# Performance work log

Measured on AMD Instinct MI355X. Metric: run time of the kernel, lower is better.

Reference implementation:

```python
import jax, jax.numpy as jnp
import numpy as np
from jax import lax

N = 40       # num_users
K = 20       # num_channels
F = 3        # num_features (conv length dim)
SS = K * N   # state_size = 800
B = 16384


def _conv1d(x, w, b):
    # x: [B, C_in, L], w: [C_out, C_in, 3], SAME padding (pad=1)
    y = lax.conv_general_dilated(x, w, window_strides=(1,), padding=[(1, 1)],
                                 dimension_numbers=('NCH', 'OIH', 'NCH'))
    return y + b[None, :, None]


def _get_mask(state):
    # state: [B, SS, F]; status feature is index 2 (== -1 since F=3)
    visited = state[:, :, 2] != 0.0                      # [B, SS]
    vm = visited.reshape(B, K, N)                        # [B, K, N] (flat idx = chan*N + user)
    user_any = vm.any(axis=1)                            # [B, N]: user visited on any channel
    chan_full = vm.sum(axis=2) >= 2                      # [B, K]: channel has >=2 users
    mask = visited \
        | jnp.broadcast_to(user_any[:, None, :], (B, K, N)).reshape(B, SS) \
        | jnp.broadcast_to(chan_full[:, :, None], (B, K, N)).reshape(B, SS)
    return mask


def setup_inputs() -> dict:
    key = jax.random.key(0)
    ks = jax.random.split(key, 12)
    state = jax.random.normal(ks[0], (B, SS, F), jnp.float32)
    keep = jax.random.bernoulli(ks[1], 0.02, (B, SS)).astype(jnp.float32)
    state = state.at[:, :, 2].multiply(keep)
    s = 0.02
    w1 = jax.random.normal(ks[2], (128, SS, 3), jnp.float32) * s
    b1 = jnp.zeros((128,), jnp.float32)
    w2 = jax.random.normal(ks[3], (256, 128, 3), jnp.float32) * s
    b2 = jnp.zeros((256,), jnp.float32)
    w3 = jax.random.normal(ks[4], (128, 256, 3), jnp.float32) * s
    b3 = jnp.zeros((128,), jnp.float32)
    wl1 = jax.random.normal(ks[5], (64 * F, 128 * F), jnp.float32) * s   # [192, 384]
    bl1 = jnp.zeros((64 * F,), jnp.float32)
    wl2 = jax.random.normal(ks[6], (SS, 64 * F), jnp.float32) * s        # [800, 192]
    bl2 = jnp.zeros((SS,), jnp.float32)
    return {"state": state, "w1": w1, "b1": b1, "w2": w2, "b2": b2,
            "w3": w3, "b3": b3, "wl1": wl1, "bl1": bl1, "wl2": wl2, "bl2": bl2}


def reference(state, w1, b1, w2, b2, w3, b3, wl1, bl1, wl2, bl2):
    mask = _get_mask(state)
    x = jax.nn.relu(_conv1d(state, w1, b1))   # [B,128,3]
    x = jax.nn.relu(_conv1d(x, w2, b2))       # [B,256,3]
    x = jax.nn.relu(_conv1d(x, w3, b3))       # [B,128,3]
    x = x.reshape(B, -1)                      # [B,384]
    x = jax.nn.relu(x @ wl1.T + bl1)          # [B,192]
    out = x @ wl2.T + bl2                     # [B,800]
    return jnp.where(mask, -jnp.inf, out)
```

## Files before the change

kernel.cpp:

```cpp
#include <hip/hip_runtime.h>
#include <cstdint>
#include <cstddef>
#include <math.h>

typedef short bf16x8 __attribute__((ext_vector_type(8)));
typedef float f32x4 __attribute__((ext_vector_type(4)));
typedef unsigned long long u64;

#define NEG_HUGE (-3.0e38f)

__device__ __forceinline__ ushort f2bf(float x) {
    union { float f; uint32_t u; } a; a.f = x;
    uint32_t r = a.u + 0x7FFF + ((a.u >> 16) & 1);
    return (ushort)(r >> 16);
}

__device__ __forceinline__ void gload_lds16(const void* g, void* l) {
    __builtin_amdgcn_global_load_lds(
        (const __attribute__((address_space(1))) uint32_t*)g,
        (__attribute__((address_space(3))) uint32_t*)l, 16, 0, 0);
}

#define SCHED() __builtin_amdgcn_sched_barrier(0)
#define SBAR() do { SCHED(); __builtin_amdgcn_s_barrier(); SCHED(); } while (0)

__device__ __forceinline__ ushort conv_elem(const float* __restrict__ w,
                                            int Cin, int idx, int Kpad) {
    int n = idx / Kpad, k = idx - n * Kpad;
    float val = 0.f;
    if (k < Cin * 3) {
        int co = n / 3, l = n % 3, ci = k / 3, lx = k % 3;
        int t = lx - l + 1;
        if (t >= 0 && t < 3) val = w[(co * Cin + ci) * 3 + t];
    }
    return f2bf(val);
}

__device__ __forceinline__ ushort lin_elem(const float* __restrict__ wl,
                                           int K, int Nreal, int idx) {
    int n = idx / K, k = idx - n * K;
    return (n < Nreal) ? f2bf(wl[n * K + k]) : (ushort)0;
}

__global__ void prep_all(const float* __restrict__ w1, const float* __restrict__ w2,
                         const float* __restrict__ w3, const float* __restrict__ wl1,
                         const float* __restrict__ wl2,
                         ushort* __restrict__ W1T, ushort* __restrict__ W2T,
                         ushort* __restrict__ W3T, ushort* __restrict__ WL1T,
                         ushort* __restrict__ WL2T) {
    int idx = blockIdx.x * 256 + threadIdx.x;
    if (idx < 933888) {
        W1T[idx] = conv_elem(w1, 800, idx, 2432);
        return;
    }
    idx -= 933888;
    if (idx < 294912) {
        W2T[idx] = conv_elem(w2, 128, idx, 384);
        return;
    }
    idx -= 294912;
    if (idx < 294912) {
        W3T[idx] = conv_elem(w3, 256, idx, 768);
        return;
    }
    idx -= 294912;
    if (idx < 73728) {
        WL1T[idx] = lin_elem(wl1, 384, 192, idx);
        return;
    }
    idx -= 73728;
    if (idx < 184320) {
        WL2T[idx] = lin_elem(wl2, 192, 800, idx);
    }
}

__global__ __launch_bounds__(512, 4)
void conv1_kernel(const float* __restrict__ state, const ushort* __restrict__ W1T,
                  const float* __restrict__ b1, ushort* __restrict__ X1g,
                  uint32_t* __restrict__ maskg)
{
    extern __shared__ char lds[];
    char* BF0 = lds;
    char* BF1 = lds + 8192;
    char* Wb0 = lds + 16384;
    char* Wb1 = lds + 40960;
    uint32_t* maskw = (uint32_t*)(lds + 65536);

    const int tid = threadIdx.x, lane = tid & 63, wid = tid >> 6;
    const int m0 = blockIdx.x * 64;
    const int n0 = blockIdx.y * 192;
    const bool domask = (blockIdx.y == 0);
    const int ml = lane & 15, kq = lane >> 4;
    const int mbase = (wid >> 2) * 32;
    const int wn0 = (wid & 3) * 48;

    const int srow = tid >> 3, seg = tid & 7;
    const float* sbase = state + (size_t)(m0 + srow) * 2400 + seg * 8;

    f32x4 acc[3][2];
    #pragma unroll
    for (int f = 0; f < 3; ++f)
        #pragma unroll
        for (int mi = 0; mi < 2; ++mi) acc[f][mi] = (f32x4){0.f, 0.f, 0.f, 0.f};

    auto loadS = [&](float4 (&sv)[2], int c) {
        int kb = c * 64 + seg * 8;
        if (kb < 2400) {
            sv[0] = *(const float4*)(sbase + c * 64);
            sv[1] = *(const float4*)(sbase + c * 64 + 4);
        } else {
            sv[0] = (float4){0.f, 0.f, 0.f, 0.f};
            sv[1] = (float4){0.f, 0.f, 0.f, 0.f};
        }
    };
    auto stage_write = [&](float4 (&sv)[2], int c, char* dst) {
        float fv[8] = {sv[0].x, sv[0].y, sv[0].z, sv[0].w,
                       sv[1].x, sv[1].y, sv[1].z, sv[1].w};
        bf16x8 h;
        #pragma unroll
        for (int j = 0; j < 8; ++j) h[j] = (short)f2bf(fv[j]);
        *(bf16x8*)(dst + srow * 128 + ((seg * 16) ^ ((srow & 7) << 4))) = h;
        if (domask) {
            int kbase = c * 64 + seg * 8;
            int kmod = kbase % 3;
            uint32_t* mrow = &maskw[srow * 25];
            #define MCHK(J) { if (fv[J] != 0.0f) { int a = (kbase + (J)) / 3; \
                              atomicOr(&mrow[a >> 5], 1u << (a & 31)); } }
            if (kmod == 0)      { MCHK(2) MCHK(5) }
            else if (kmod == 1) { MCHK(1) MCHK(4) MCHK(7) }
            else                { MCHK(0) MCHK(3) MCHK(6) }
            #undef MCHK
        }
    };
    auto loadW = [&](int c, char* dst) {
        #pragma unroll
        for (int i = 0; i < 3; ++i) {
            int s = i * 512 + tid;
            int r = s >> 3, o8 = s & 7;
            gload_lds16(W1T + (size_t)(n0 + r) * 2432 + c * 64 + ((o8 ^ (r & 7)) * 8),
                        dst + s * 16);
        }
    };
    auto mfmaC = [&](const char* wb, const char* sb) {
        #pragma unroll
        for (int ks = 0; ks < 2; ++ks) {
            bf16x8 af[3], bv[2];
            #pragma unroll
            for (int f = 0; f < 3; ++f) {
                int n = wn0 + f * 16 + ml;
                af[f] = *(const bf16x8*)(wb + n * 128 + (((ks * 4 + kq) * 16) ^ ((n & 7) << 4)));
            }
            #pragma unroll
            for (int mi = 0; mi < 2; ++mi) {
                int m = mbase + mi * 16 + ml;
                bv[mi] = *(const bf16x8*)(sb + m * 128 + (((ks * 4 + kq) * 16) ^ ((m & 7) << 4)));
            }
            #pragma unroll
            for (int f = 0; f < 3; ++f)
                #pragma unroll
                for (int mi = 0; mi < 2; ++mi)
                    acc[f][mi] = __builtin_amdgcn_mfma_f32_16x16x32_bf16(af[f], bv[mi], acc[f][mi], 0, 0, 0);
        }
    };

    for (int i = tid; i < 64 * 25; i += 512) maskw[i] = 0;
    float4 svA[2], svB[2];
    loadS(svA, 0);
    loadW(0, Wb0);
    loadS(svB, 1);
    SCHED();
    asm volatile("s_waitcnt lgkmcnt(0)" ::: "memory");
    SBAR();

    #define BODY(SV, C, SB, WBC, WBN) do {                                   \
        stage_write(SV, (C), SB);                                            \
        SCHED();                                                             \
        asm volatile("s_waitcnt lgkmcnt(0)" ::: "memory");                   \
        SBAR();                                                              \
        loadW(((C) + 1 > 37) ? 37 : (C) + 1, WBN);                           \
        loadS(SV, ((C) + 2 > 37) ? 37 : (C) + 2);                            \
        SCHED();                                                             \
        asm volatile("s_waitcnt vmcnt(7)" ::: "memory");                     \
        SBAR();                                                              \
        mfmaC(WBC, SB);                                                      \
    } while (0)

    #pragma unroll 1
    for (int p = 0; p < 19; ++p) {
        BODY(svA, 2 * p,     BF0, Wb0, Wb1);
        BODY(svB, 2 * p + 1, BF1, Wb1, Wb0);
    }
    #undef BODY

    asm volatile("s_waitcnt vmcnt(0) lgkmcnt(0)" ::: "memory");
    SBAR();

    {
        const int nq4 = (lane >> 4) * 4;
        #pragma unroll
        for (int f = 0; f < 3; ++f) {
            int n4 = n0 + wn0 + f * 16 + nq4;
            float bv0 = b1[n4 / 3], bv1 = b1[(n4 + 1) / 3];
            float bv2 = b1[(n4 + 2) / 3], bv3 = b1[(n4 + 3) / 3];
            #pragma unroll
            for (int mi = 0; mi < 2; ++mi) {
                int m = mbase + mi * 16 + ml;
                ushort4 o;
                o.x = f2bf(fmaxf(acc[f][mi][0] + bv0, 0.f));
                o.y = f2bf(fmaxf(acc[f][mi][1] + bv1, 0.f));
                o.z = f2bf(fmaxf(acc[f][mi][2] + bv2, 0.f));
                o.w = f2bf(fmaxf(acc[f][mi][3] + bv3, 0.f));
                *(ushort4*)(X1g + (size_t)(m0 + m) * 384 + n4) = o;
            }
        }
    }

    if (domask && tid < 64) {
        uint32_t* mw = &maskw[tid * 25];
        const u64 M40 = (1ull << 40) - 1;
        u64 ua = 0; uint32_t cf = 0;
        #pragma unroll
        for (int g = 0; g < 5; ++g) {
            uint32_t w0 = mw[5*g], w1 = mw[5*g+1], w2 = mw[5*g+2], w3 = mw[5*g+3], w4 = mw[5*g+4];
            u64 c0 = ( (u64)w0        | ((u64)w1 << 32)) & M40;
            u64 c1 = (((u64)w1 >> 8)  | ((u64)w2 << 24)) & M40;
            u64 c2 = (((u64)w2 >> 16) | ((u64)w3 << 16)) & M40;
            u64 c3 = (((u64)w3 >> 24) | ((u64)w4 << 8))  & M40;
            ua |= c0 | c1 | c2 | c3;
            if (__popcll(c0) >= 2) cf |= 1u << (4*g);
            if (__popcll(c1) >= 2) cf |= 1u << (4*g+1);
            if (__popcll(c2) >= 2) cf |= 1u << (4*g+2);
            if (__popcll(c3) >= 2) cf |= 1u << (4*g+3);
        }
        uint32_t* mg = maskg + (size_t)(m0 + tid) * 25;
        #pragma unroll
        for (int g = 0; g < 5; ++g) {
            uint32_t w0 = mw[5*g], w1 = mw[5*g+1], w2 = mw[5*g+2], w3 = mw[5*g+3], w4 = mw[5*g+4];
            u64 c0 = ( (u64)w0        | ((u64)w1 << 32)) & M40;
            u64 c1 = (((u64)w1 >> 8)  | ((u64)w2 << 24)) & M40;
            u64 c2 = (((u64)w2 >> 16) | ((u64)w3 << 16)) & M40;
            u64 c3 = (((u64)w3 >> 24) | ((u64)w4 << 8))  & M40;
            u64 m0v = c0 | ua | (((cf >> (4*g))     & 1u) ? M40 : 0ull);
            u64 m1v = c1 | ua | (((cf >> (4*g + 1)) & 1u) ? M40 : 0ull);
            u64 m2v = c2 | ua | (((cf >> (4*g + 2)) & 1u) ? M40 : 0ull);
            u64 m3v = c3 | ua | (((cf >> (4*g + 3)) & 1u) ? M40 : 0ull);
            mg[5*g]   = (uint32_t)m0v;
            mg[5*g+1] = (uint32_t)(m0v >> 32) | (uint32_t)(m1v << 8);
            mg[5*g+2] = (uint32_t)(m1v >> 24) | (uint32_t)(m2v << 16);
            mg[5*g+3] = (uint32_t)(m2v >> 16) | (uint32_t)(m3v << 24);
            mg[5*g+4] = (uint32_t)(m3v >> 8);
        }
    }
}

template<int K, bool BDIV3, bool RELU, bool F32OUT>
__global__ __launch_bounds__(512, 4)
void glayer3(const ushort* __restrict__ Ag, const ushort* __restrict__ WTg,
             const float* __restrict__ bias, void* __restrict__ Yg, int ldy,
             const uint32_t* __restrict__ maskg)
{
    constexpr int MF = 4, NF = 3;
    constexpr int MT = 128, NT = 192;
    constexpr int NC = K / 64;
    constexpr int ABYTES = MT * 128;
    constexpr int WBYTES = NT * 128;
    static_assert(NC >= 3, "pipeline assumes >=3 chunks");
    extern __shared__ char lds[];

    const int tid = threadIdx.x, lane = tid & 63, wid = tid >> 6;
    const int m0 = blockIdx.x * MT;
    const int n0 = blockIdx.y * NT;
    const int ml = lane & 15, kq = lane >> 4;
    const int mw = wid >> 2, nw = wid & 3;
    const int mbase = mw * MF * 16;
    const int wn0 = nw * NF * 16;

    f32x4 acc[NF][MF];
    #pragma unroll
    for (int f = 0; f < NF; ++f)
        #pragma unroll
        for (int mi = 0; mi < MF; ++mi) acc[f][mi] = (f32x4){0.f, 0.f, 0.f, 0.f};

    auto stage = [&](int c, int b) {
        char* Ab = lds + b * ABYTES;
        char* Wb = lds + 2 * ABYTES + b * WBYTES;
        #pragma unroll
        for (int i = 0; i < 2; ++i) {
            int s = i * 512 + tid;
            int r = s >> 3, o8 = s & 7;
            gload_lds16(Ag + (size_t)(m0 + r) * K + c * 64 + ((o8 ^ (r & 7)) * 8),
                        Ab + s * 16);
        }
        #pragma unroll
        for (int i = 0; i < 3; ++i) {
            int s = i * 512 + tid;
            int r = s >> 3, o8 = s & 7;
            gload_lds16(WTg + (size_t)(n0 + r) * K + c * 64 + ((o8 ^ (r & 7)) * 8),
                        Wb + s * 16);
        }
    };
    auto mfmaC = [&](int b) {
        const char* Ab = lds + b * ABYTES;
        const char* Wb = lds + 2 * ABYTES + b * WBYTES;
        #pragma unroll
        for (int ks = 0; ks < 2; ++ks) {
            bf16x8 af[NF], bv[MF];
            #pragma unroll
            for (int f = 0; f < NF; ++f) {
                int n = wn0 + f * 16 + ml;
                af[f] = *(const bf16x8*)(Wb + n * 128 + (((ks * 4 + kq) * 16) ^ ((n & 7) << 4)));
            }
            #pragma unroll
            for (int mi = 0; mi < MF; ++mi) {
                int m = mbase + mi * 16 + ml;
                bv[mi] = *(const bf16x8*)(Ab + m * 128 + (((ks * 4 + kq) * 16) ^ ((m & 7) << 4)));
            }
            #pragma unroll
            for (int f = 0; f < NF; ++f)
                #pragma unroll
                for (int mi = 0; mi < MF; ++mi)
                    acc[f][mi] = __builtin_amdgcn_mfma_f32_16x16x32_bf16(af[f], bv[mi], acc[f][mi], 0, 0, 0);
        }
    };

    stage(0, 0);
    stage(1, 1);
    asm volatile("s_waitcnt vmcnt(5)" ::: "memory");
    SBAR();

    #pragma unroll 1
    for (int c = 0; c < NC; ++c) {
        mfmaC(c & 1);
        if (c + 2 < NC) {
            SBAR();
            stage(c + 2, c & 1);
            asm volatile("s_waitcnt vmcnt(5)" ::: "memory");
            SBAR();
        } else if (c + 1 < NC) {
            SBAR();
            asm volatile("s_waitcnt vmcnt(0)" ::: "memory");
            SBAR();
        }
    }

    const int nq4 = (lane >> 4) * 4;
    if (!F32OUT) {
        ushort* Y = (ushort*)Yg;
        #pragma unroll
        for (int f = 0; f < NF; ++f) {
            int n4 = n0 + wn0 + f * 16 + nq4;
            float bv0 = bias[BDIV3 ? n4 / 3 : n4];
            float bv1 = bias[BDIV3 ? (n4 + 1) / 3 : n4 + 1];
            float bv2 = bias[BDIV3 ? (n4 + 2) / 3 : n4 + 2];
            float bv3 = bias[BDIV3 ? (n4 + 3) / 3 : n4 + 3];
            #pragma unroll
            for (int mi = 0; mi < MF; ++mi) {
                int m = mbase + mi * 16 + ml;
                float x0 = acc[f][mi][0] + bv0, x1 = acc[f][mi][1] + bv1;
                float x2 = acc[f][mi][2] + bv2, x3 = acc[f][mi][3] + bv3;
                if (RELU) { x0 = fmaxf(x0, 0.f); x1 = fmaxf(x1, 0.f);
                            x2 = fmaxf(x2, 0.f); x3 = fmaxf(x3, 0.f); }
                ushort4 o = {f2bf(x0), f2bf(x1), f2bf(x2), f2bf(x3)};
                *(ushort4*)(Y + (size_t)(m0 + m) * ldy + n4) = o;
            }
        }
    } else {
        float* Y = (float*)Yg;
        #pragma unroll
        for (int f = 0; f < NF; ++f) {
            int nf = n0 + wn0 + f * 16;
            if (nf < 800) {
                int n4 = nf + nq4, sh = n4 & 31;
                float bv0 = bias[n4], bv1 = bias[n4 + 1];
                float bv2 = bias[n4 + 2], bv3 = bias[n4 + 3];
                #pragma unroll
                for (int mi = 0; mi < MF; ++mi) {
                    int m = mbase + mi * 16 + ml;
                    uint32_t mwv = maskg[(size_t)(m0 + m) * 25 + (nf >> 5)];
                    float4 v;
                    v.x = ((mwv >> (sh + 0)) & 1u) ? NEG_HUGE : (acc[f][mi][0] + bv0);
                    v.y = ((mwv >> (sh + 1)) & 1u) ? NEG_HUGE : (acc[f][mi][1] + bv1);
                    v.z = ((mwv >> (sh + 2)) & 1u) ? NEG_HUGE : (acc[f][mi][2] + bv2);
                    v.w = ((mwv >> (sh + 3)) & 1u) ? NEG_HUGE : (acc[f][mi][3] + bv3);
                    *(float4*)(Y + (size_t)(m0 + m) * ldy + n4) = v;
                }
            }
        }
    }
}

__global__ void ws_fail_kernel(float* out) {
    if (threadIdx.x == 0 && blockIdx.x == 0) out[0] = NAN;
}

extern "C" void kernel_launch(void* const* d_in, const int* in_sizes, int n_in,
                              void* d_out, int out_size, void* d_ws, size_t ws_size,
                              hipStream_t stream) {
    const float* state = (const float*)d_in[0];
    const float* w1  = (const float*)d_in[1];
    const float* b1  = (const float*)d_in[2];
    const float* w2  = (const float*)d_in[3];
    const float* b2  = (const float*)d_in[4];
    const float* w3  = (const float*)d_in[5];
    const float* b3  = (const float*)d_in[6];
    const float* wl1 = (const float*)d_in[7];
    const float* bl1 = (const float*)d_in[8];
    const float* wl2 = (const float*)d_in[9];
    const float* bl2 = (const float*)d_in[10];
    float* out = (float*)d_out;

    char* ws = (char*)d_ws;
    size_t off = 0;
    auto carve = [&](size_t bytes) {
        char* p = ws + off;
        off = (off + bytes + 255) & ~(size_t)255;
        return p;
    };
    ushort* W1T  = (ushort*)carve(384ull * 2432 * 2);
    ushort* W2T  = (ushort*)carve(768ull * 384 * 2);
    ushort* W3T  = (ushort*)carve(384ull * 768 * 2);
    ushort* WL1T = (ushort*)carve(192ull * 384 * 2);
    ushort* WL2T = (ushort*)carve(960ull * 192 * 2);
    ushort* X1g  = (ushort*)carve(16384ull * 384 * 2);
    ushort* X2g  = (ushort*)carve(16384ull * 768 * 2);
    ushort* X3g  = (ushort*)carve(16384ull * 384 * 2);
    ushort* X4g  = (ushort*)carve(16384ull * 192 * 2);
    uint32_t* maskg = (uint32_t*)carve(16384ull * 25 * 4);

    if (off > ws_size) {
        ws_fail_kernel<<<1, 64, 0, stream>>>(out);
        return;
    }

    prep_all<<<(1781760 + 255) / 256, 256, 0, stream>>>(w1, w2, w3, wl1, wl2,
                                                        W1T, W2T, W3T, WL1T, WL2T);

    (void)hipFuncSetAttribute(reinterpret_cast<const void*>(conv1_kernel),
                        hipFuncAttributeMaxDynamicSharedMemorySize, 71936);
    conv1_kernel<<<dim3(256, 2), 512, 71936, stream>>>(state, W1T, b1, X1g, maskg);

    auto kc2 = glayer3<384, true, true, false>;
    (void)hipFuncSetAttribute(reinterpret_cast<const void*>(kc2),
                        hipFuncAttributeMaxDynamicSharedMemorySize, 81920);
    kc2<<<dim3(128, 4), 512, 81920, stream>>>(X1g, W2T, b2, X2g, 768, nullptr);

    auto kc3 = glayer3<768, true, true, false>;
    (void)hipFuncSetAttribute(reinterpret_cast<const void*>(kc3),
                        hipFuncAttributeMaxDynamicSharedMemorySize, 81920);
    kc3<<<dim3(128, 2), 512, 81920, stream>>>(X2g, W3T, b3, X3g, 384, nullptr);

    auto kc4 = glayer3<384, false, true, false>;
    (void)hipFuncSetAttribute(reinterpret_cast<const void*>(kc4),
                        hipFuncAttributeMaxDynamicSharedMemorySize, 81920);
    kc4<<<dim3(128, 1), 512, 81920, stream>>>(X3g, WL1T, bl1, X4g, 192, nullptr);

    auto kc5 = glayer3<192, false, false, true>;
    (void)hipFuncSetAttribute(reinterpret_cast<const void*>(kc5),
                        hipFuncAttributeMaxDynamicSharedMemorySize, 81920);
    kc5<<<dim3(128, 5), 512, 81920, stream>>>(X4g, WL2T, bl2, out, 800, maskg);
}
```

Baseline: 132.6 us.

## Shrink conv1 N-tile to 128 and move mask finalization into layer-2 kernel

Conv1's output tile shrinks from 192 to 128 columns, so the grid grows to three column blocks, the LDS footprint drops to 48KB and the occupancy hint rises to 6 blocks per CU. The per-block LDS mask staging is removed: mask bits are OR'd atomically straight into global memory, which prep_all now zeroes. The user-any and channel-full finalization moves into the epilogue of the conv2 kernel. This lowers conv1 register and LDS pressure and raises parallelism, at the cost of global atomics in place of LDS atomics and an extra pass over W1T tiles.

```diff
diff --git a/kernel.cpp b/kernel.cpp
--- a/kernel.cpp
+++ b/kernel.cpp
@@ -47,34 +47,22 @@
                          const float* __restrict__ wl2,
                          ushort* __restrict__ W1T, ushort* __restrict__ W2T,
                          ushort* __restrict__ W3T, ushort* __restrict__ WL1T,
-                         ushort* __restrict__ WL2T) {
+                         ushort* __restrict__ WL2T, uint32_t* __restrict__ maskg) {
     int idx = blockIdx.x * 256 + threadIdx.x;
-    if (idx < 933888) {
-        W1T[idx] = conv_elem(w1, 800, idx, 2432);
-        return;
-    }
+    if (idx < 933888) { W1T[idx] = conv_elem(w1, 800, idx, 2432); return; }
     idx -= 933888;
-    if (idx < 294912) {
-        W2T[idx] = conv_elem(w2, 128, idx, 384);
-        return;
-    }
+    if (idx < 294912) { W2T[idx] = conv_elem(w2, 128, idx, 384); return; }
     idx -= 294912;
-    if (idx < 294912) {
-        W3T[idx] = conv_elem(w3, 256, idx, 768);
-        return;
-    }
+    if (idx < 294912) { W3T[idx] = conv_elem(w3, 256, idx, 768); return; }
     idx -= 294912;
-    if (idx < 73728) {
-        WL1T[idx] = lin_elem(wl1, 384, 192, idx);
-        return;
-    }
+    if (idx < 73728)  { WL1T[idx] = lin_elem(wl1, 384, 192, idx); return; }
     idx -= 73728;
-    if (idx < 184320) {
-        WL2T[idx] = lin_elem(wl2, 192, 800, idx);
-    }
-}
-
-__global__ __launch_bounds__(512, 4)
+    if (idx < 184320) { WL2T[idx] = lin_elem(wl2, 192, 800, idx); return; }
+    idx -= 184320;
+    if (idx < 409600) maskg[idx] = 0;
+}
+
+__global__ __launch_bounds__(512, 6)
 void conv1_kernel(const float* __restrict__ state, const ushort* __restrict__ W1T,
                   const float* __restrict__ b1, ushort* __restrict__ X1g,
                   uint32_t* __restrict__ maskg)
@@ -83,23 +71,22 @@
     char* BF0 = lds;
     char* BF1 = lds + 8192;
     char* Wb0 = lds + 16384;
-    char* Wb1 = lds + 40960;
-    uint32_t* maskw = (uint32_t*)(lds + 65536);
+    char* Wb1 = lds + 32768;
 
     const int tid = threadIdx.x, lane = tid & 63, wid = tid >> 6;
     const int m0 = blockIdx.x * 64;
-    const int n0 = blockIdx.y * 192;
+    const int n0 = blockIdx.y * 128;
     const bool domask = (blockIdx.y == 0);
     const int ml = lane & 15, kq = lane >> 4;
     const int mbase = (wid >> 2) * 32;
-    const int wn0 = (wid & 3) * 48;
+    const int wn0 = (wid & 3) * 32;
 
     const int srow = tid >> 3, seg = tid & 7;
     const float* sbase = state + (size_t)(m0 + srow) * 2400 + seg * 8;
 
-    f32x4 acc[3][2];
+    f32x4 acc[2][2];
     #pragma unroll
-    for (int f = 0; f < 3; ++f)
+    for (int f = 0; f < 2; ++f)
         #pragma unroll
         for (int mi = 0; mi < 2; ++mi) acc[f][mi] = (f32x4){0.f, 0.f, 0.f, 0.f};
 
@@ -123,7 +110,7 @@
         if (domask) {
             int kbase = c * 64 + seg * 8;
             int kmod = kbase % 3;
-            uint32_t* mrow = &maskw[srow * 25];
+            uint32_t* mrow = maskg + (size_t)(m0 + srow) * 25;
             #define MCHK(J) { if (fv[J] != 0.0f) { int a = (kbase + (J)) / 3; \
                               atomicOr(&mrow[a >> 5], 1u << (a & 31)); } }
             if (kmod == 0)      { MCHK(2) MCHK(5) }
@@ -134,7 +121,7 @@
     };
     auto loadW = [&](int c, char* dst) {
         #pragma unroll
-        for (int i = 0; i < 3; ++i) {
+        for (int i = 0; i < 2; ++i) {
             int s = i * 512 + tid;
             int r = s >> 3, o8 = s & 7;
             gload_lds16(W1T + (size_t)(n0 + r) * 2432 + c * 64 + ((o8 ^ (r & 7)) * 8),
@@ -144,9 +131,9 @@
     auto mfmaC = [&](const char* wb, const char* sb) {
         #pragma unroll
         for (int ks = 0; ks < 2; ++ks) {
-            bf16x8 af[3], bv[2];
-            #pragma unroll
-            for (int f = 0; f < 3; ++f) {
+            bf16x8 af[2], bv[2];
+            #pragma unroll
+            for (int f = 0; f < 2; ++f) {
                 int n = wn0 + f * 16 + ml;
                 af[f] = *(const bf16x8*)(wb + n * 128 + (((ks * 4 + kq) * 16) ^ ((n & 7) << 4)));
             }
@@ -156,14 +143,13 @@
                 bv[mi] = *(const bf16x8*)(sb + m * 128 + (((ks * 4 + kq) * 16) ^ ((m & 7) << 4)));
             }
             #pragma unroll
-            for (int f = 0; f < 3; ++f)
+            for (int f = 0; f < 2; ++f)
                 #pragma unroll
                 for (int mi = 0; mi < 2; ++mi)
                     acc[f][mi] = __builtin_amdgcn_mfma_f32_16x16x32_bf16(af[f], bv[mi], acc[f][mi], 0, 0, 0);
         }
     };
 
-    for (int i = tid; i < 64 * 25; i += 512) maskw[i] = 0;
     float4 svA[2], svB[2];
     loadS(svA, 0);
     loadW(0, Wb0);
@@ -180,7 +166,7 @@
         loadW(((C) + 1 > 37) ? 37 : (C) + 1, WBN);                           \
         loadS(SV, ((C) + 2 > 37) ? 37 : (C) + 2);                            \
         SCHED();                                                             \
-        asm volatile("s_waitcnt vmcnt(7)" ::: "memory");                     \
+        asm volatile("s_waitcnt vmcnt(6)" ::: "memory");                     \
         SBAR();                                                              \
         mfmaC(WBC, SB);                                                      \
     } while (0)
@@ -198,7 +184,7 @@
     {
         const int nq4 = (lane >> 4) * 4;
         #pragma unroll
-        for (int f = 0; f < 3; ++f) {
+        for (int f = 0; f < 2; ++f) {
             int n4 = n0 + wn0 + f * 16 + nq4;
             float bv0 = b1[n4 / 3], bv1 = b1[(n4 + 1) / 3];
             float bv2 = b1[(n4 + 2) / 3], bv3 = b1[(n4 + 3) / 3];
@@ -214,50 +200,13 @@
             }
         }
     }
-
-    if (domask && tid < 64) {
-        uint32_t* mw = &maskw[tid * 25];
-        const u64 M40 = (1ull << 40) - 1;
-        u64 ua = 0; uint32_t cf = 0;
-        #pragma unroll
-        for (int g = 0; g < 5; ++g) {
-            uint32_t w0 = mw[5*g], w1 = mw[5*g+1], w2 = mw[5*g+2], w3 = mw[5*g+3], w4 = mw[5*g+4];
-            u64 c0 = ( (u64)w0        | ((u64)w1 << 32)) & M40;
-            u64 c1 = (((u64)w1 >> 8)  | ((u64)w2 << 24)) & M40;
-            u64 c2 = (((u64)w2 >> 16) | ((u64)w3 << 16)) & M40;
-            u64 c3 = (((u64)w3 >> 24) | ((u64)w4 << 8))  & M40;
-            ua |= c0 | c1 | c2 | c3;
-            if (__popcll(c0) >= 2) cf |= 1u << (4*g);
-            if (__popcll(c1) >= 2) cf |= 1u << (4*g+1);
-            if (__popcll(c2) >= 2) cf |= 1u << (4*g+2);
-            if (__popcll(c3) >= 2) cf |= 1u << (4*g+3);
-        }
-        uint32_t* mg = maskg + (size_t)(m0 + tid) * 25;
-        #pragma unroll
-        for (int g = 0; g < 5; ++g) {
-            uint32_t w0 = mw[5*g], w1 = mw[5*g+1], w2 = mw[5*g+2], w3 = mw[5*g+3], w4 = mw[5*g+4];
-            u64 c0 = ( (u64)w0        | ((u64)w1 << 32)) & M40;
-            u64 c1 = (((u64)w1 >> 8)  | ((u64)w2 << 24)) & M40;
-            u64 c2 = (((u64)w2 >> 16) | ((u64)w3 << 16)) & M40;
-            u64 c3 = (((u64)w3 >> 24) | ((u64)w4 << 8))  & M40;
-            u64 m0v = c0 | ua | (((cf >> (4*g))     & 1u) ? M40 : 0ull);
-            u64 m1v = c1 | ua | (((cf >> (4*g + 1)) & 1u) ? M40 : 0ull);
-            u64 m2v = c2 | ua | (((cf >> (4*g + 2)) & 1u) ? M40 : 0ull);
-            u64 m3v = c3 | ua | (((cf >> (4*g + 3)) & 1u) ? M40 : 0ull);
-            mg[5*g]   = (uint32_t)m0v;
-            mg[5*g+1] = (uint32_t)(m0v >> 32) | (uint32_t)(m1v << 8);
-            mg[5*g+2] = (uint32_t)(m1v >> 24) | (uint32_t)(m2v << 16);
-            mg[5*g+3] = (uint32_t)(m2v >> 16) | (uint32_t)(m3v << 24);
-            mg[5*g+4] = (uint32_t)(m3v >> 8);
-        }
-    }
 }
 
 template<int K, bool BDIV3, bool RELU, bool F32OUT>
 __global__ __launch_bounds__(512, 4)
 void glayer3(const ushort* __restrict__ Ag, const ushort* __restrict__ WTg,
              const float* __restrict__ bias, void* __restrict__ Yg, int ldy,
-             const uint32_t* __restrict__ maskg)
+             const uint32_t* __restrict__ maskg, uint32_t* __restrict__ fin_mask)
 {
     constexpr int MF = 4, NF = 3;
     constexpr int MT = 128, NT = 192;
@@ -387,6 +336,45 @@
             }
         }
     }
+
+    if (fin_mask && blockIdx.y == 0 && tid < 128) {
+        uint32_t* mw = fin_mask + (size_t)(m0 + tid) * 25;
+        uint32_t w[25];
+        #pragma unroll
+        for (int i = 0; i < 25; ++i) w[i] = mw[i];
+        const u64 M40 = (1ull << 40) - 1;
+        u64 ua = 0; uint32_t cf = 0;
+        #pragma unroll
+        for (int g = 0; g < 5; ++g) {
+            uint32_t w0 = w[5*g], w1 = w[5*g+1], w2 = w[5*g+2], w3 = w[5*g+3], w4 = w[5*g+4];
+            u64 c0 = ( (u64)w0        | ((u64)w1 << 32)) & M40;
+            u64 c1 = (((u64)w1 >> 8)  | ((u64)w2 << 24)) & M40;
+            u64 c2 = (((u64)w2 >> 16) | ((u64)w3 << 16)) & M40;
+            u64 c3 = (((u64)w3 >> 24) | ((u64)w4 << 8))  & M40;
+            ua |= c0 | c1 | c2 | c3;
+            if (__popcll(c0) >= 2) cf |= 1u << (4*g);
+            if (__popcll(c1) >= 2) cf |= 1u << (4*g+1);
+            if (__popcll(c2) >= 2) cf |= 1u << (4*g+2);
+            if (__popcll(c3) >= 2) cf |= 1u << (4*g+3);
+        }
+        #pragma unroll
+        for (int g = 0; g < 5; ++g) {
+            uint32_t w0 = w[5*g], w1 = w[5*g+1], w2 = w[5*g+2], w3 = w[5*g+3], w4 = w[5*g+4];
+            u64 c0 = ( (u64)w0        | ((u64)w1 << 32)) & M40;
+            u64 c1 = (((u64)w1 >> 8)  | ((u64)w2 << 24)) & M40;
+            u64 c2 = (((u64)w2 >> 16) | ((u64)w3 << 16)) & M40;
+            u64 c3 = (((u64)w3 >> 24) | ((u64)w4 << 8))  & M40;
+            u64 m0v = c0 | ua | (((cf >> (4*g))     & 1u) ? M40 : 0ull);
+            u64 m1v = c1 | ua | (((cf >> (4*g + 1)) & 1u) ? M40 : 0ull);
+            u64 m2v = c2 | ua | (((cf >> (4*g + 2)) & 1u) ? M40 : 0ull);
+            u64 m3v = c3 | ua | (((cf >> (4*g + 3)) & 1u) ? M40 : 0ull);
+            mw[5*g]   = (uint32_t)m0v;
+            mw[5*g+1] = (uint32_t)(m0v >> 32) | (uint32_t)(m1v << 8);
+            mw[5*g+2] = (uint32_t)(m1v >> 24) | (uint32_t)(m2v << 16);
+            mw[5*g+3] = (uint32_t)(m2v >> 16) | (uint32_t)(m3v << 24);
+            mw[5*g+4] = (uint32_t)(m3v >> 8);
+        }
+    }
 }
 
 __global__ void ws_fail_kernel(float* out) {
@@ -432,30 +420,30 @@
         return;
     }
 
-    prep_all<<<(1781760 + 255) / 256, 256, 0, stream>>>(w1, w2, w3, wl1, wl2,
-                                                        W1T, W2T, W3T, WL1T, WL2T);
+    prep_all<<<(2191360 + 255) / 256, 256, 0, stream>>>(w1, w2, w3, wl1, wl2,
+                                                        W1T, W2T, W3T, WL1T, WL2T, maskg);
 
     (void)hipFuncSetAttribute(reinterpret_cast<const void*>(conv1_kernel),
-                        hipFuncAttributeMaxDynamicSharedMemorySize, 71936);
-    conv1_kernel<<<dim3(256, 2), 512, 71936, stream>>>(state, W1T, b1, X1g, maskg);
+                        hipFuncAttributeMaxDynamicSharedMemorySize, 49152);
+    conv1_kernel<<<dim3(256, 3), 512, 49152, stream>>>(state, W1T, b1, X1g, maskg);
 
     auto kc2 = glayer3<384, true, true, false>;
     (void)hipFuncSetAttribute(reinterpret_cast<const void*>(kc2),
                         hipFuncAttributeMaxDynamicSharedMemorySize, 81920);
-    kc2<<<dim3(128, 4), 512, 81920, stream>>>(X1g, W2T, b2, X2g, 768, nullptr);
+    kc2<<<dim3(128, 4), 512, 81920, stream>>>(X1g, W2T, b2, X2g, 768, nullptr, maskg);
 
     auto kc3 = glayer3<768, true, true, false>;
     (void)hipFuncSetAttribute(reinterpret_cast<const void*>(kc3),
                         hipFuncAttributeMaxDynamicSharedMemorySize, 81920);
-    kc3<<<dim3(128, 2), 512, 81920, stream>>>(X2g, W3T, b3, X3g, 384, nullptr);
+    kc3<<<dim3(128, 2), 512, 81920, stream>>>(X2g, W3T, b3, X3g, 384, nullptr, nullptr);
 
     auto kc4 = glayer3<384, false, true, false>;
     (void)hipFuncSetAttribute(reinterpret_cast<const void*>(kc4),
                         hipFuncAttributeMaxDynamicSharedMemorySize, 81920);
-    kc4<<<dim3(128, 1), 512, 81920, stream>>>(X3g, WL1T, bl1, X4g, 192, nullptr);
+    kc4<<<dim3(128, 1), 512, 81920, stream>>>(X3g, WL1T, bl1, X4g, 192, nullptr, nullptr);
 
     auto kc5 = glayer3<192, false, false, true>;
     (void)hipFuncSetAttribute(reinterpret_cast<const void*>(kc5),
                         hipFuncAttributeMaxDynamicSharedMemorySize, 81920);
-    kc5<<<dim3(128, 5), 512, 81920, stream>>>(X4g, WL2T, bl2, out, 800, maskg);
-}
+    kc5<<<dim3(128, 5), 512, 81920, stream>>>(X4g, WL2T, bl2, out, 800, maskg, nullptr);
+}
```

After: 149.9 us. +13.0%, slower.
